# Optimization experiments

Hardware: AMD Instinct MI355X
Metric: run time of the kernel (lower is better)

Reference implementation:

```python
import jax, jax.numpy as jnp
import numpy as np

B, S, D, H, DFF = 2, 2048, 1024, 16, 4096
DK = D // H
EPS = 1e-6


def layer_norm(x, alpha, bias):
    # torch: alpha * (x - mean) / (std_unbiased + eps) + bias
    mean = jnp.mean(x, axis=-1, keepdims=True)
    std = jnp.sqrt(jnp.var(x, axis=-1, keepdims=True, ddof=1))
    return alpha * (x - mean) / (std + EPS) + bias


def setup_inputs() -> dict:
    key = jax.random.key(0)
    ks = jax.random.split(key, 10)
    w = lambda k, shape: (jax.random.normal(k, shape, jnp.float32) * 0.02)
    return {
        "x": jax.random.normal(ks[0], (B, S, D), jnp.float32),
        "mask": jnp.ones((B, 1, 1, S), jnp.int32),
        "wq": w(ks[1], (D, D)),
        "wk": w(ks[2], (D, D)),
        "wv": w(ks[3], (D, D)),
        "wo": w(ks[4], (D, D)),
        "w1": w(ks[5], (DFF, D)),
        "b1": jnp.zeros((DFF,), jnp.float32),
        "w2": w(ks[6], (D, DFF)),
        "b2": jnp.zeros((D,), jnp.float32),
        "alpha1": jnp.ones((D,), jnp.float32),
        "bias1": jnp.zeros((D,), jnp.float32),
        "alpha2": jnp.ones((D,), jnp.float32),
        "bias2": jnp.zeros((D,), jnp.float32),
    }


def reference(x, mask, wq, wk, wv, wo, w1, b1, w2, b2, alpha1, bias1, alpha2, bias2):
    # --- residual 1: pre-norm + self-attention ---
    xn = layer_norm(x, alpha1, bias1)                      # [B,S,D]
    q = (xn @ wq.T).reshape(B, S, H, DK).transpose(0, 2, 1, 3)  # [B,H,S,DK]
    k = (xn @ wk.T).reshape(B, S, H, DK).transpose(0, 2, 1, 3)
    v = (xn @ wv.T).reshape(B, S, H, DK).transpose(0, 2, 1, 3)
    scores = jnp.einsum("bhqd,bhkd->bhqk", q, k) / jnp.sqrt(jnp.float32(DK))
    scores = jnp.where(mask == 0, jnp.float32(-1e9), scores)
    attn = jax.nn.softmax(scores, axis=-1)                 # [B,H,S,S]
    av = jnp.einsum("bhqk,bhkd->bhqd", attn, v)            # [B,H,S,DK]
    av = av.transpose(0, 2, 1, 3).reshape(B, S, D)
    x = x + av @ wo.T                                      # dropout p=0
    # --- residual 2: pre-norm + FFN ---
    xn2 = layer_norm(x, alpha2, bias2)
    h = jax.nn.relu(xn2 @ w1.T + b1)                       # [B,S,DFF]
    x = x + h @ w2.T + b2
    return x
```

## Files before the change

### kernel.cpp

```cpp
#include <hip/hip_runtime.h>

#define B_   2
#define S_   2048
#define D_   1024
#define H_   16
#define DK_  64
#define DFF_ 4096
#define NTOK (B_ * S_)

#define QSCALE 0.18033688011112042f

typedef __bf16 bf16x8 __attribute__((ext_vector_type(8)));
typedef __bf16 bf16x4 __attribute__((ext_vector_type(4)));
typedef float  f32x4  __attribute__((ext_vector_type(4)));

#if __has_builtin(__builtin_amdgcn_exp2f)
#define EXP2(x) __builtin_amdgcn_exp2f(x)
#else
#define EXP2(x) exp2f(x)
#endif

__device__ __forceinline__ void ld16(const __bf16* g, __bf16* l) {
  __builtin_amdgcn_global_load_lds(
      (const __attribute__((address_space(1))) void*)g,
      (__attribute__((address_space(3))) void*)l, 16, 0, 0);
}

#define RAW_BAR()     __asm__ __volatile__("s_barrier" ::: "memory")
#define SCHED_FENCE() __builtin_amdgcn_sched_barrier(0)

__device__ __forceinline__ void xcd_swizzle(int& bx, int& by) {
  const int gx = gridDim.x;
  const int flat = blockIdx.y * gx + blockIdx.x;
  const int x = flat & 7;
  const int n = flat >> 3;
  if (gx == 32) {
    const int px = (x & 1) << 4, py = (x >> 1) << 3;
    const int g = n >> 5, rem = n & 31;
    bx = px + (g << 2) + (rem & 3);
    by = py + (rem >> 2);
  } else {
    const int g = n >> 4, rem = n & 15;
    bx = (g << 2) + (rem & 3);
    by = (x << 2) + (rem >> 2);
  }
}

__device__ __forceinline__ void xcd_swz256(int& bx, int& by) {
  const int gx = gridDim.x;
  const int flat = blockIdx.y * gx + blockIdx.x;
  const int x = flat & 7, n = flat >> 3;
  if (gx == 16) { by = ((x >> 1) << 2) + (n >> 3); bx = ((x & 1) << 3) + (n & 7); }
  else          { by = (x << 1) + (n >> 2);        bx = n & 3; }
}

__device__ __forceinline__ void lda4(bf16x8 (&afr)[4], const __bf16* hb,
                                     int abase, int f0) {
#pragma unroll
  for (int i = 0; i < 4; ++i)
    afr[i] = *(const bf16x8*)(hb + abase + (f0 + i) * 512);
}

__device__ __forceinline__ void ldb4(bf16x8 (&bfr)[4], const __bf16* hb,
                                     int bbase) {
#pragma unroll
  for (int j = 0; j < 4; ++j)
    bfr[j] = *(const bf16x8*)(hb + bbase + j * 512);
}

__device__ __forceinline__ void mm16(f32x4 (&acc)[8][4], const bf16x8 (&afr)[4],
                                     const bf16x8 (&bfr)[4], int r0) {
#pragma unroll
  for (int i = 0; i < 4; ++i)
#pragma unroll
    for (int j = 0; j < 4; ++j)
      acc[r0 + i][j] =
          __builtin_amdgcn_mfma_f32_16x16x32_bf16(afr[i], bfr[j], acc[r0 + i][j], 0, 0, 0);
}

__device__ __forceinline__ void gemm_core_256(
    const __bf16* __restrict__ A, const __bf16* __restrict__ W,
    int ld, int kLen, int rowA0, int rowW0,
    f32x4 (&acc)[8][4], __bf16* Ls)
{
  const int t = threadIdx.x;
  const int lane = t & 63, wv = t >> 6;
  const int wm = wv >> 2, wn = wv & 3;
  const int l15 = lane & 15, q4 = lane >> 4;

  const int lane_rd = l15 * 32 + ((q4 * 8) ^ (((l15 >> 1) & 3) << 3));
  const int abase = wm * 4096 + lane_rd;
  const int bbase = wn * 2048 + lane_rd;

  const int sc0 = t ^ ((t >> 3) & 3);
  const __bf16* gA0 = A + (size_t)(rowA0 + (sc0 >> 2)) * ld + (sc0 & 3) * 8;
  const __bf16* gA1 = gA0 + (size_t)128 * ld;
  const __bf16* gW0 = W + (size_t)(rowW0 + (sc0 >> 2)) * ld + (sc0 & 3) * 8;
  const __bf16* gW1 = gW0 + (size_t)128 * ld;
  const int d0 = wv * 512, d1 = 4096 + wv * 512;

#pragma unroll
  for (int i = 0; i < 8; ++i)
#pragma unroll
    for (int j = 0; j < 4; ++j) acc[i][j] = (f32x4){0.f, 0.f, 0.f, 0.f};

#define HBASE(slot, mat, h) (Ls + ((((slot)*2) + (mat)) * 2 + (h)) * 8192)
#define STG_A(tt, h, slot) do { __bf16* _d = HBASE(slot, 0, h);              \
    const int _ko = (tt) * 64 + (h) * 32;                                    \
    ld16(gA0 + _ko, _d + d0); ld16(gA1 + _ko, _d + d1); } while (0)
#define STG_B(tt, h, slot) do { __bf16* _d = HBASE(slot, 1, h);              \
    const int _ko = (tt) * 64 + (h) * 32;                                    \
    ld16(gW0 + _ko, _d + d0); ld16(gW1 + _ko, _d + d1); } while (0)
#define MFMA_PH(r0) do { RAW_BAR(); SCHED_FENCE();                           \
    __builtin_amdgcn_s_setprio(1); mm16(acc, afr, bfr, r0);                  \
    __builtin_amdgcn_s_setprio(0); SCHED_FENCE(); RAW_BAR(); } while (0)

  const int NT = kLen >> 6;
  bf16x8 afr[4], bfr[4];

  STG_A(0, 0, 0); STG_A(0, 1, 0); STG_B(0, 0, 0); STG_B(0, 1, 0);
  STG_B(1, 0, 1); STG_A(1, 0, 1); STG_B(1, 1, 1);
  __asm__ __volatile__("s_waitcnt vmcnt(6)" ::: "memory");
  RAW_BAR(); SCHED_FENCE();

  for (int u = 0; u < NT; u += 2) {
    const bool g2 = (u + 2) < NT, g3 = (u + 3) < NT;
    lda4(afr, HBASE(0, 0, 0), abase, 0); ldb4(bfr, HBASE(0, 1, 0), bbase);
    STG_A(u + 1, 1, 1);
    MFMA_PH(0);
    lda4(afr, HBASE(0, 0, 0), abase, 4);
    if (g2) STG_B(u + 2, 0, 0);
    MFMA_PH(4);
    lda4(afr, HBASE(0, 0, 1), abase, 0); ldb4(bfr, HBASE(0, 1, 1), bbase);
    if (g2) STG_A(u + 2, 0, 0);
    MFMA_PH(0);
    lda4(afr, HBASE(0, 0, 1), abase, 4);
    if (g2) {
      STG_B(u + 2, 1, 0);
      __asm__ __volatile__("s_waitcnt vmcnt(6)" ::: "memory");
    } else {
      __asm__ __volatile__("s_waitcnt vmcnt(0)" ::: "memory");
    }
    MFMA_PH(4);
    lda4(afr, HBASE(1, 0, 0), abase, 0); ldb4(bfr, HBASE(1, 1, 0), bbase);
    if (g2) STG_A(u + 2, 1, 0);
    MFMA_PH(0);
    lda4(afr, HBASE(1, 0, 0), abase, 4);
    if (g3) STG_B(u + 3, 0, 1);
    MFMA_PH(4);
    lda4(afr, HBASE(1, 0, 1), abase, 0); ldb4(bfr, HBASE(1, 1, 1), bbase);
    if (g3) STG_A(u + 3, 0, 1);
    MFMA_PH(0);
    lda4(afr, HBASE(1, 0, 1), abase, 4);
    if (g3) STG_B(u + 3, 1, 1);
    __asm__ __volatile__("s_waitcnt vmcnt(6)" ::: "memory");
    MFMA_PH(4);
  }
#undef HBASE
#undef STG_A
#undef STG_B
#undef MFMA_PH
}

__device__ __forceinline__ void gemm_core_128(
    const __bf16* __restrict__ A, const __bf16* __restrict__ W,
    int ld, int kLen, int rowA0, int rowW0,
    f32x4 (&acc)[4][4], __bf16* As, __bf16* Bs)
{
  const int t    = threadIdx.x;
  const int lane = t & 63;
  const int wv   = t >> 6;
  const int wm   = (wv >> 1) << 6;
  const int wn   = (wv & 1) << 6;
  const int l15  = lane & 15;
  const int q4   = lane >> 4;

#pragma unroll
  for (int i = 0; i < 4; ++i)
#pragma unroll
    for (int j = 0; j < 4; ++j)
      acc[i][j] = (f32x4){0.f, 0.f, 0.f, 0.f};

  const __bf16* gA = A + (size_t)(rowA0 + 32 * wv + l15) * ld + q4 * 8;
  const __bf16* gW = W + (size_t)(rowW0 + 32 * wv + l15) * ld + q4 * 8;
  __bf16* lA = As + wv * 2048;
  __bf16* lB = Bs + wv * 2048;
  const size_t r16 = (size_t)16 * ld;

  const int fbg = (q4 << 7) + (l15 << 3);
  const int ia = (wm >> 4);
  const int ib = (wn >> 4);

  for (int k0 = 0; k0 < kLen; k0 += 64) {
    ld16(gA + k0,            lA);
    ld16(gA + k0 + 32,       lA + 512);
    ld16(gA + k0 + r16,      lA + 1024);
    ld16(gA + k0 + r16 + 32, lA + 1536);
    ld16(gW + k0,            lB);
    ld16(gW + k0 + 32,       lB + 512);
    ld16(gW + k0 + r16,      lB + 1024);
    ld16(gW + k0 + r16 + 32, lB + 1536);
    __syncthreads();
#pragma unroll
    for (int s = 0; s < 2; ++s) {
      bf16x8 af[4], bw[4];
#pragma unroll
      for (int i = 0; i < 4; ++i)
        af[i] = *(const bf16x8*)(As + (ia + i) * 1024 + s * 512 + fbg);
#pragma unroll
      for (int j = 0; j < 4; ++j)
        bw[j] = *(const bf16x8*)(Bs + (ib + j) * 1024 + s * 512 + fbg);
#pragma unroll
      for (int i = 0; i < 4; ++i)
#pragma unroll
        for (int j = 0; j < 4; ++j)
          acc[i][j] = __builtin_amdgcn_mfma_f32_16x16x32_bf16(af[i], bw[j], acc[i][j], 0, 0, 0);
    }
    __syncthreads();
  }
}

__global__ __launch_bounds__(512, 2) void gemm_qkv_256(
    const __bf16* __restrict__ xn,
    const __bf16* __restrict__ wqb, const __bf16* __restrict__ wkb,
    const __bf16* __restrict__ wvb,
    __bf16* __restrict__ qo, __bf16* __restrict__ ko, __bf16* __restrict__ vto)
{
  __shared__ __align__(16) __bf16 Ls[65536];
  int bx, by; xcd_swz256(bx, by);
  const __bf16* W = blockIdx.z == 0 ? wqb : (blockIdx.z == 1 ? wkb : wvb);
  f32x4 acc[8][4];
  gemm_core_256(xn, W, D_, D_, by * 256, bx * 256, acc, Ls);

  const int t = threadIdx.x, lane = t & 63, wv = t >> 6;
  const int wm = wv >> 2, wn = wv & 3;
  const int l15 = lane & 15, q4 = lane >> 4;
  const int row0 = by * 256 + wm * 128;
  const int col0 = bx * 256 + wn * 64;

  if (blockIdx.z < 2) {
    __bf16* o = blockIdx.z == 0 ? qo : ko;
    const float sc = blockIdx.z == 0 ? QSCALE : 1.0f;
#pragma unroll
    for (int fr = 0; fr < 8; ++fr)
#pragma unroll
      for (int fc = 0; fc < 4; ++fc) {
        const int col = col0 + fc * 16 + l15;
#pragma unroll
        for (int r = 0; r < 4; ++r) {
          const int row = row0 + fr * 16 + q4 * 4 + r;
          o[(size_t)row * D_ + col] = (__bf16)(acc[fr][fc][r] * sc);
        }
      }
  } else {
#pragma unroll
    for (int fr = 0; fr < 8; ++fr)
#pragma unroll
      for (int fc = 0; fc < 4; ++fc) {
        const int tok0 = row0 + fr * 16 + q4 * 4;
        const int c    = col0 + fc * 16 + l15;
        const int b0 = tok0 >> 11, s0 = tok0 & (S_ - 1);
        const int hh = c >> 6, dd = c & (DK_ - 1);
        bf16x4 pk;
#pragma unroll
        for (int r = 0; r < 4; ++r) pk[r] = (__bf16)acc[fr][fc][r];
        *(bf16x4*)&vto[(size_t)((b0 * H_ + hh) * DK_ + dd) * S_ + s0] = pk;
      }
  }
}

__global__ __launch_bounds__(512, 2) void gemm_ffn1_256(
    const __bf16* __restrict__ A, const __bf16* __restrict__ W,
    __bf16* __restrict__ outb, const float* __restrict__ bias)
{
  __shared__ __align__(16) __bf16 Ls[65536];
  int bx, by; xcd_swz256(bx, by);
  f32x4 acc[8][4];
  gemm_core_256(A, W, D_, D_, by * 256, bx * 256, acc, Ls);

  const int t = threadIdx.x, lane = t & 63, wv = t >> 6;
  const int wm = wv >> 2, wn = wv & 3;
  const int l15 = lane & 15, q4 = lane >> 4;
  const int row0 = by * 256 + wm * 128;
  const int col0 = bx * 256 + wn * 64;

#pragma unroll
  for (int fr = 0; fr < 8; ++fr)
#pragma unroll
    for (int fc = 0; fc < 4; ++fc) {
      const int col = col0 + fc * 16 + l15;
      const float bs = bias[col];
#pragma unroll
      for (int r = 0; r < 4; ++r) {
        const int row = row0 + fr * 16 + q4 * 4 + r;
        outb[(size_t)row * DFF_ + col] = (__bf16)fmaxf(acc[fr][fc][r] + bs, 0.0f);
      }
    }
}

__global__ __launch_bounds__(512, 2) void gemm_ffn2_sk4(
    const __bf16* __restrict__ A, const __bf16* __restrict__ W,
    __bf16* __restrict__ pp)
{
  __shared__ __align__(16) __bf16 Ls[65536];
  int bx, by; xcd_swz256(bx, by);
  const int z = blockIdx.z;
  f32x4 acc[8][4];
  gemm_core_256(A + (size_t)z * 1024, W + (size_t)z * 1024, DFF_, 1024,
                by * 256, bx * 256, acc, Ls);

  const int t = threadIdx.x, lane = t & 63, wv = t >> 6;
  const int wm = wv >> 2, wn = wv & 3;
  const int l15 = lane & 15, q4 = lane >> 4;
  const int row0 = by * 256 + wm * 128;
  const int col0 = bx * 256 + wn * 64;
  __bf16* out = pp + (size_t)z * NTOK * D_;

#pragma unroll
  for (int fr = 0; fr < 8; ++fr)
#pragma unroll
    for (int fc = 0; fc < 4; ++fc) {
      const int col = col0 + fc * 16 + l15;
#pragma unroll
      for (int r = 0; r < 4; ++r) {
        const int row = row0 + fr * 16 + q4 * 4 + r;
        out[(size_t)row * D_ + col] = (__bf16)acc[fr][fc][r];
      }
    }
}

__global__ __launch_bounds__(256) void gemm_splitk_f32(
    const __bf16* __restrict__ A, const __bf16* __restrict__ W,
    int K, int kPart, float* __restrict__ pp)
{
  __shared__ __align__(16) __bf16 As[128 * 64];
  __shared__ __align__(16) __bf16 Bs[128 * 64];
  int bx, by; xcd_swizzle(bx, by);
  f32x4 acc[4][4];
  const int z = blockIdx.z;
  gemm_core_128(A + (size_t)z * kPart, W + (size_t)z * kPart, K, kPart,
                by * 128, bx * 128, acc, As, Bs);

  const int t = threadIdx.x, lane = t & 63, wv = t >> 6;
  const int wm = (wv >> 1) << 6, wn = (wv & 1) << 6;
  const int l15 = lane & 15, q4 = lane >> 4;
  const int row0 = by * 128 + wm;
  const int col0 = bx * 128 + wn;
  float* out = pp + (size_t)z * NTOK * D_;

#pragma unroll
  for (int i = 0; i < 4; ++i)
#pragma unroll
    for (int j = 0; j < 4; ++j)
#pragma unroll
      for (int r = 0; r < 4; ++r) {
        int row = row0 + 16 * i + q4 * 4 + r;
        int col = col0 + 16 * j + l15;
        out[(size_t)row * D_ + col] = acc[i][j][r];
      }
}

__global__ __launch_bounds__(256) void oproj_ln_reduce(
    const float* __restrict__ x, const float* __restrict__ p0,
    const float* __restrict__ p1, const float* __restrict__ alpha,
    const float* __restrict__ bias, float* __restrict__ x1,
    __bf16* __restrict__ xn2)
{
  const int row = blockIdx.x;
  const int t = threadIdx.x;
  const size_t base = (size_t)row * D_;
  float4 v  = ((const float4*)(x  + base))[t];
  const float4 a0 = ((const float4*)(p0 + base))[t];
  const float4 a1 = ((const float4*)(p1 + base))[t];
  v.x += a0.x + a1.x; v.y += a0.y + a1.y;
  v.z += a0.z + a1.z; v.w += a0.w + a1.w;
  ((float4*)(x1 + base))[t] = v;

  float s  = v.x + v.y + v.z + v.w;
  float ss = v.x * v.x + v.y * v.y + v.z * v.z + v.w * v.w;
#pragma unroll
  for (int m = 1; m < 64; m <<= 1) {
    s  += __shfl_xor(s, m);
    ss += __shfl_xor(ss, m);
  }
  __shared__ float red[8];
  if ((t & 63) == 0) { red[t >> 6] = s; red[4 + (t >> 6)] = ss; }
  __syncthreads();
  s  = red[0] + red[1] + red[2] + red[3];
  ss = red[4] + red[5] + red[6] + red[7];
  const float mean = s * (1.0f / D_);
  float var = (ss - (float)D_ * mean * mean) * (1.0f / (D_ - 1));
  var = fmaxf(var, 0.0f);
  const float inv = 1.0f / (sqrtf(var) + 1e-6f);
  const float4 al = ((const float4*)alpha)[t];
  const float4 bi = ((const float4*)bias)[t];
  bf16x4 o;
  o.x = (__bf16)(al.x * (v.x - mean) * inv + bi.x);
  o.y = (__bf16)(al.y * (v.y - mean) * inv + bi.y);
  o.z = (__bf16)(al.z * (v.z - mean) * inv + bi.z);
  o.w = (__bf16)(al.w * (v.w - mean) * inv + bi.w);
  ((bf16x4*)(xn2 + base))[t] = o;
}

__global__ __launch_bounds__(256) void ffn2_reduce(
    const float* __restrict__ x1, const __bf16* __restrict__ pp,
    const float* __restrict__ b2, float* __restrict__ out)
{
  const int idx4 = blockIdx.x * 256 + threadIdx.x;
  float4 v = ((const float4*)x1)[idx4];
  const float4 bs = ((const float4*)b2)[idx4 & 255];
  const size_t st = (size_t)NTOK * D_ / 4;
  const bf16x4 q0 = ((const bf16x4*)pp)[idx4];
  const bf16x4 q1 = ((const bf16x4*)pp)[idx4 + st];
  const bf16x4 q2 = ((const bf16x4*)pp)[idx4 + 2 * st];
  const bf16x4 q3 = ((const bf16x4*)pp)[idx4 + 3 * st];
  v.x += bs.x + (float)q0[0] + (float)q1[0] + (float)q2[0] + (float)q3[0];
  v.y += bs.y + (float)q0[1] + (float)q1[1] + (float)q2[1] + (float)q3[1];
  v.z += bs.z + (float)q0[2] + (float)q1[2] + (float)q2[2] + (float)q3[2];
  v.w += bs.w + (float)q0[3] + (float)q1[3] + (float)q2[3] + (float)q3[3];
  ((float4*)out)[idx4] = v;
}

struct CastJobs {
  const float* src[6];
  __bf16* dst[6];
  int n4[6];
};

__global__ __launch_bounds__(256) void cast_ln_kernel(
    CastJobs cj, const float* __restrict__ x, const float* __restrict__ alpha,
    const float* __restrict__ bias, __bf16* __restrict__ xn1)
{
  const int j = blockIdx.y;
  if (j < 6) {
    const int i = blockIdx.x * 256 + threadIdx.x;
    if (i < cj.n4[j]) {
      float4 v = ((const float4*)cj.src[j])[i];
      bf16x4 o;
      o.x = (__bf16)v.x; o.y = (__bf16)v.y; o.z = (__bf16)v.z; o.w = (__bf16)v.w;
      ((bf16x4*)cj.dst[j])[i] = o;
    }
    return;
  }
  const int row = blockIdx.x;
  const int t = threadIdx.x;
  const float4 v = ((const float4*)(x + (size_t)row * D_))[t];
  float s  = v.x + v.y + v.z + v.w;
  float ss = v.x * v.x + v.y * v.y + v.z * v.z + v.w * v.w;
#pragma unroll
  for (int m = 1; m < 64; m <<= 1) {
    s  += __shfl_xor(s, m);
    ss += __shfl_xor(ss, m);
  }
  __shared__ float red[8];
  if ((t & 63) == 0) { red[t >> 6] = s; red[4 + (t >> 6)] = ss; }
  __syncthreads();
  s  = red[0] + red[1] + red[2] + red[3];
  ss = red[4] + red[5] + red[6] + red[7];
  const float mean = s * (1.0f / D_);
  float var = (ss - (float)D_ * mean * mean) * (1.0f / (D_ - 1));
  var = fmaxf(var, 0.0f);
  const float inv = 1.0f / (sqrtf(var) + 1e-6f);
  const float4 al = ((const float4*)alpha)[t];
  const float4 bi = ((const float4*)bias)[t];
  bf16x4 o;
  o.x = (__bf16)(al.x * (v.x - mean) * inv + bi.x);
  o.y = (__bf16)(al.y * (v.y - mean) * inv + bi.y);
  o.z = (__bf16)(al.z * (v.z - mean) * inv + bi.z);
  o.w = (__bf16)(al.w * (v.w - mean) * inv + bi.w);
  ((bf16x4*)(xn1 + (size_t)row * D_))[t] = o;
}

__global__ __launch_bounds__(256) void attn_kernel(
    const __bf16* __restrict__ qg, const __bf16* __restrict__ kg,
    const __bf16* __restrict__ vtg, const int* __restrict__ mask,
    __bf16* __restrict__ av)
{
  __shared__ __align__(16) __bf16 Ks[64 * 64];
  __shared__ __align__(16) __bf16 Vt[64 * 64];
  __shared__ __align__(16) __bf16 Ps[128 * 72];

  const int t = threadIdx.x, lane = t & 63, wv = t >> 6;
  const int l15 = lane & 15, q4 = lane >> 4;
  const int bh = blockIdx.x;
  const int b = bh >> 4, h = bh & (H_ - 1);
  const int q0 = blockIdx.y * 128;

  const int srow = lane & 7, sc8 = lane >> 3;
  const __bf16* qg0 = qg + (size_t)(b * S_ + q0 + 32 * wv + srow) * D_ + h * DK_ + sc8 * 8;
  __bf16* lQ = Ps + wv * 2304;
#pragma unroll
  for (int p = 0; p < 4; ++p)
    ld16(qg0 + (size_t)(8 * p) * D_, lQ + 512 * p);

  const __bf16* kg0 = kg + (size_t)(b * S_ + 16 * wv + srow) * D_ + h * DK_ + sc8 * 8;
  const __bf16* vt0 = vtg + (size_t)(bh * DK_ + 16 * wv + srow) * S_ + sc8 * 8;

  const int fb = ((l15 >> 3) << 9) + (q4 << 6) + ((l15 & 7) << 3);
  const int mrow = b * S_;

  float lsum[2] = {0.0f, 0.0f};
  f32x4 oacc[2][4];
#pragma unroll
  for (int m = 0; m < 2; ++m)
#pragma unroll
    for (int jd = 0; jd < 4; ++jd) oacc[m][jd] = (f32x4){0.f, 0.f, 0.f, 0.f};
  bf16x8 bq[2][2];

  for (int kv0 = 0; kv0 < S_; kv0 += 64) {
    ld16(kg0 + (size_t)kv0 * D_,       Ks + wv * 1024);
    ld16(kg0 + (size_t)(kv0 + 8) * D_, Ks + wv * 1024 + 512);
    ld16(vt0 + kv0,                    Vt + wv * 1024);
    ld16(vt0 + (size_t)8 * S_ + kv0,   Vt + wv * 1024 + 512);
    const int mv = mask[mrow + kv0 + lane];
    const bool dirty = (__ballot(mv == 0) != 0ull);
    __syncthreads();

    if (kv0 == 0) {
#pragma unroll
      for (int j = 0; j < 2; ++j)
#pragma unroll
        for (int s = 0; s < 2; ++s)
          bq[j][s] = *(const bf16x8*)(lQ + j * 1024 + s * 256 + fb);
    }

    f32x4 sacc[4][2];
#pragma unroll
    for (int i = 0; i < 4; ++i)
#pragma unroll
      for (int j = 0; j < 2; ++j) sacc[i][j] = (f32x4){0.f, 0.f, 0.f, 0.f};
#pragma unroll
    for (int i = 0; i < 4; ++i)
#pragma unroll
      for (int s = 0; s < 2; ++s) {
        bf16x8 ak = *(const bf16x8*)(Ks + i * 1024 + fb + s * 256);
#pragma unroll
        for (int j = 0; j < 2; ++j)
          sacc[i][j] = __builtin_amdgcn_mfma_f32_16x16x32_bf16(ak, bq[j][s], sacc[i][j], 0, 0, 0);
      }

    if (dirty) {
#pragma unroll
      for (int i = 0; i < 4; ++i)
#pragma unroll
        for (int r = 0; r < 4; ++r)
          if (mask[mrow + kv0 + 16 * i + 4 * q4 + r] == 0) {
            sacc[i][0][r] = -1e30f;
            sacc[i][1][r] = -1e30f;
          }
    }

#pragma unroll
    for (int j = 0; j < 2; ++j) {
      float rs = 0.0f;
#pragma unroll
      for (int i = 0; i < 4; ++i) {
        bf16x4 pb;
#pragma unroll
        for (int r = 0; r < 4; ++r) {
          float pp = EXP2(sacc[i][j][r]);
          rs += pp;
          pb[r] = (__bf16)pp;
        }
        *(bf16x4*)(Ps + (wv * 32 + j * 16 + l15) * 72 + 16 * i + q4 * 4) = pb;
      }
      lsum[j] += rs;
    }

    bf16x8 ap[2][2];
#pragma unroll
    for (int m = 0; m < 2; ++m)
#pragma unroll
      for (int s = 0; s < 2; ++s)
        ap[m][s] = *(const bf16x8*)(Ps + (wv * 32 + 16 * m + l15) * 72 + s * 32 + q4 * 8);
#pragma unroll
    for (int jd = 0; jd < 4; ++jd)
#pragma unroll
      for (int s = 0; s < 2; ++s) {
        bf16x8 bv = *(const bf16x8*)(Vt + jd * 1024 + fb + s * 256);
#pragma unroll
        for (int m = 0; m < 2; ++m)
          oacc[m][jd] = __builtin_amdgcn_mfma_f32_16x16x32_bf16(ap[m][s], bv, oacc[m][jd], 0, 0, 0);
      }
    __syncthreads();
  }

#pragma unroll
  for (int j = 0; j < 2; ++j) {
    lsum[j] += __shfl_xor(lsum[j], 16);
    lsum[j] += __shfl_xor(lsum[j], 32);
  }
  float lt[2][4];
#pragma unroll
  for (int m = 0; m < 2; ++m)
#pragma unroll
    for (int r = 0; r < 4; ++r) lt[m][r] = 1.0f / __shfl(lsum[m], q4 * 4 + r);
#pragma unroll
  for (int m = 0; m < 2; ++m)
#pragma unroll
    for (int jd = 0; jd < 4; ++jd)
#pragma unroll
      for (int r = 0; r < 4; ++r) {
        int tok = b * S_ + q0 + wv * 32 + 16 * m + q4 * 4 + r;
        int c   = h * DK_ + jd * 16 + l15;
        av[(size_t)tok * D_ + c] = (__bf16)(oacc[m][jd][r] * lt[m][r]);
      }
}

extern "C" void kernel_launch(void* const* d_in, const int* in_sizes, int n_in,
                              void* d_out, int out_size, void* d_ws, size_t ws_size,
                              hipStream_t stream) {
  const float* x      = (const float*)d_in[0];
  const int*   mask   = (const int*)d_in[1];
  const float* wq     = (const float*)d_in[2];
  const float* wk     = (const float*)d_in[3];
  const float* wv     = (const float*)d_in[4];
  const float* wo     = (const float*)d_in[5];
  const float* w1     = (const float*)d_in[6];
  const float* b1     = (const float*)d_in[7];
  const float* w2     = (const float*)d_in[8];
  const float* b2     = (const float*)d_in[9];
  const float* alpha1 = (const float*)d_in[10];
  const float* bias1  = (const float*)d_in[11];
  const float* alpha2 = (const float*)d_in[12];
  const float* bias2  = (const float*)d_in[13];

  char* ws = (char*)d_ws;
  __bf16* wqb = (__bf16*)(ws + ((size_t)0 << 20));
  __bf16* wkb = (__bf16*)(ws + ((size_t)2 << 20));
  __bf16* wvb = (__bf16*)(ws + ((size_t)4 << 20));
  __bf16* wob = (__bf16*)(ws + ((size_t)6 << 20));
  __bf16* w1b = (__bf16*)(ws + ((size_t)8 << 20));
  __bf16* w2b = (__bf16*)(ws + ((size_t)16 << 20));
  __bf16* xn1 = (__bf16*)(ws + ((size_t)24 << 20));
  __bf16* qb  = (__bf16*)(ws + ((size_t)32 << 20));
  __bf16* kb  = (__bf16*)(ws + ((size_t)40 << 20));
  __bf16* vtb = (__bf16*)(ws + ((size_t)48 << 20));
  __bf16* avb = (__bf16*)(ws + ((size_t)56 << 20));
  float*  x1  = (float*) (ws + ((size_t)64 << 20));
  __bf16* xn2 = (__bf16*)(ws + ((size_t)56 << 20));
  __bf16* hb  = (__bf16*)(ws + ((size_t)24 << 20));
  float*  op0 = (float*) (ws + ((size_t)24 << 20));
  float*  op1 = (float*) (ws + ((size_t)40 << 20));
  __bf16* fpp = (__bf16*)(ws + ((size_t)32 << 20));

  CastJobs cj;
  cj.src[0] = wq; cj.dst[0] = wqb; cj.n4[0] = D_ * D_ / 4;
  cj.src[1] = wk; cj.dst[1] = wkb; cj.n4[1] = D_ * D_ / 4;
  cj.src[2] = wv; cj.dst[2] = wvb; cj.n4[2] = D_ * D_ / 4;
  cj.src[3] = wo; cj.dst[3] = wob; cj.n4[3] = D_ * D_ / 4;
  cj.src[4] = w1; cj.dst[4] = w1b; cj.n4[4] = DFF_ * D_ / 4;
  cj.src[5] = w2; cj.dst[5] = w2b; cj.n4[5] = DFF_ * D_ / 4;

  cast_ln_kernel<<<dim3(DFF_ * D_ / 4 / 256, 7), 256, 0, stream>>>(
      cj, x, alpha1, bias1, xn1);

  gemm_qkv_256<<<dim3(D_ / 256, NTOK / 256, 3), 512, 0, stream>>>(
      xn1, wqb, wkb, wvb, qb, kb, vtb);

  attn_kernel<<<dim3(B_ * H_, S_ / 128), 256, 0, stream>>>(qb, kb, vtb, mask, avb);

  gemm_splitk_f32<<<dim3(D_ / 128, NTOK / 128, 2), 256, 0, stream>>>(
      avb, wob, D_, D_ / 2, op0);

  oproj_ln_reduce<<<dim3(NTOK), 256, 0, stream>>>(
      x, op0, op1, alpha2, bias2, x1, xn2);

  gemm_ffn1_256<<<dim3(DFF_ / 256, NTOK / 256), 512, 0, stream>>>(
      xn2, w1b, hb, b1);

  gemm_ffn2_sk4<<<dim3(D_ / 256, NTOK / 256, 4), 512, 0, stream>>>(
      hb, w2b, fpp);

  ffn2_reduce<<<dim3(NTOK * D_ / 4 / 256), 256, 0, stream>>>(
      x1, fpp, b2, (float*)d_out);
}
```

Measured before the change: 332.8 us.

## Double-buffer K/V tiles in attention and precompute per-tile mask flags

The attention kernel now keeps two shared-memory buffers each for K and V. The next KV tile's global-to-LDS loads are issued before the current tile's MFMA work, so loading overlaps compute instead of stalling at a barrier every iteration. The per-tile 'any mask zero' check is computed once up front into a small shared array, replacing a per-iteration mask load and ballot. s_setprio is also raised around the MFMA blocks. The cost is doubled K/V LDS usage, which may reduce occupancy.

```diff
diff --git a/kernel.cpp b/kernel.cpp
--- a/kernel.cpp
+++ b/kernel.cpp
@@ -476,9 +476,10 @@
     const __bf16* __restrict__ vtg, const int* __restrict__ mask,
     __bf16* __restrict__ av)
 {
-  __shared__ __align__(16) __bf16 Ks[64 * 64];
-  __shared__ __align__(16) __bf16 Vt[64 * 64];
+  __shared__ __align__(16) __bf16 Ks[2][64 * 64];
+  __shared__ __align__(16) __bf16 Vt[2][64 * 64];
   __shared__ __align__(16) __bf16 Ps[128 * 72];
+  __shared__ int Dd[32];
 
   const int t = threadIdx.x, lane = t & 63, wv = t >> 6;
   const int l15 = lane & 15, q4 = lane >> 4;
@@ -496,32 +497,49 @@
   const __bf16* kg0 = kg + (size_t)(b * S_ + 16 * wv + srow) * D_ + h * DK_ + sc8 * 8;
   const __bf16* vt0 = vtg + (size_t)(bh * DK_ + 16 * wv + srow) * S_ + sc8 * 8;
 
+  if (t < 32) Dd[t] = 0;
+
+  ld16(kg0,                  Ks[0] + wv * 1024);
+  ld16(kg0 + (size_t)8 * D_, Ks[0] + wv * 1024 + 512);
+  ld16(vt0,                  Vt[0] + wv * 1024);
+  ld16(vt0 + (size_t)8 * S_, Vt[0] + wv * 1024 + 512);
+
+  __syncthreads();
+
+  {
+    const int4* m4 = (const int4*)(mask + (size_t)b * S_) + t * 2;
+    const int4 a = m4[0], c = m4[1];
+    const bool anyz = (a.x == 0) | (a.y == 0) | (a.z == 0) | (a.w == 0) |
+                      (c.x == 0) | (c.y == 0) | (c.z == 0) | (c.w == 0);
+    if (anyz) Dd[t >> 3] = 1;
+  }
+  __syncthreads();
+
   const int fb = ((l15 >> 3) << 9) + (q4 << 6) + ((l15 & 7) << 3);
   const int mrow = b * S_;
 
+  bf16x8 bq[2][2];
+#pragma unroll
+  for (int j = 0; j < 2; ++j)
+#pragma unroll
+    for (int s = 0; s < 2; ++s)
+      bq[j][s] = *(const bf16x8*)(lQ + j * 1024 + s * 256 + fb);
+
   float lsum[2] = {0.0f, 0.0f};
   f32x4 oacc[2][4];
 #pragma unroll
   for (int m = 0; m < 2; ++m)
 #pragma unroll
     for (int jd = 0; jd < 4; ++jd) oacc[m][jd] = (f32x4){0.f, 0.f, 0.f, 0.f};
-  bf16x8 bq[2][2];
 
   for (int kv0 = 0; kv0 < S_; kv0 += 64) {
-    ld16(kg0 + (size_t)kv0 * D_,       Ks + wv * 1024);
-    ld16(kg0 + (size_t)(kv0 + 8) * D_, Ks + wv * 1024 + 512);
-    ld16(vt0 + kv0,                    Vt + wv * 1024);
-    ld16(vt0 + (size_t)8 * S_ + kv0,   Vt + wv * 1024 + 512);
-    const int mv = mask[mrow + kv0 + lane];
-    const bool dirty = (__ballot(mv == 0) != 0ull);
-    __syncthreads();
-
-    if (kv0 == 0) {
-#pragma unroll
-      for (int j = 0; j < 2; ++j)
-#pragma unroll
-        for (int s = 0; s < 2; ++s)
-          bq[j][s] = *(const bf16x8*)(lQ + j * 1024 + s * 256 + fb);
+    const int buf = (kv0 >> 6) & 1;
+    if (kv0 + 64 < S_) {
+      const size_t nk = (size_t)(kv0 + 64);
+      ld16(kg0 + nk * D_,              Ks[buf ^ 1] + wv * 1024);
+      ld16(kg0 + (nk + 8) * D_,        Ks[buf ^ 1] + wv * 1024 + 512);
+      ld16(vt0 + nk,                   Vt[buf ^ 1] + wv * 1024);
+      ld16(vt0 + (size_t)8 * S_ + nk,  Vt[buf ^ 1] + wv * 1024 + 512);
     }
 
     f32x4 sacc[4][2];
@@ -529,17 +547,19 @@
     for (int i = 0; i < 4; ++i)
 #pragma unroll
       for (int j = 0; j < 2; ++j) sacc[i][j] = (f32x4){0.f, 0.f, 0.f, 0.f};
+    __builtin_amdgcn_s_setprio(1);
 #pragma unroll
     for (int i = 0; i < 4; ++i)
 #pragma unroll
       for (int s = 0; s < 2; ++s) {
-        bf16x8 ak = *(const bf16x8*)(Ks + i * 1024 + fb + s * 256);
+        bf16x8 ak = *(const bf16x8*)(Ks[buf] + i * 1024 + fb + s * 256);
 #pragma unroll
         for (int j = 0; j < 2; ++j)
           sacc[i][j] = __builtin_amdgcn_mfma_f32_16x16x32_bf16(ak, bq[j][s], sacc[i][j], 0, 0, 0);
       }
-
-    if (dirty) {
+    __builtin_amdgcn_s_setprio(0);
+
+    if (Dd[kv0 >> 6]) {
 #pragma unroll
       for (int i = 0; i < 4; ++i)
 #pragma unroll
@@ -573,15 +593,18 @@
 #pragma unroll
       for (int s = 0; s < 2; ++s)
         ap[m][s] = *(const bf16x8*)(Ps + (wv * 32 + 16 * m + l15) * 72 + s * 32 + q4 * 8);
+    __builtin_amdgcn_s_setprio(1);
 #pragma unroll
     for (int jd = 0; jd < 4; ++jd)
 #pragma unroll
       for (int s = 0; s < 2; ++s) {
-        bf16x8 bv = *(const bf16x8*)(Vt + jd * 1024 + fb + s * 256);
+        bf16x8 bv = *(const bf16x8*)(Vt[buf] + jd * 1024 + fb + s * 256);
 #pragma unroll
         for (int m = 0; m < 2; ++m)
           oacc[m][jd] = __builtin_amdgcn_mfma_f32_16x16x32_bf16(ap[m][s], bv, oacc[m][jd], 0, 0, 0);
       }
+    __builtin_amdgcn_s_setprio(0);
+
     __syncthreads();
   }
 
```

Result: faster. 326.1 us (-2.0%).
